# Kernel tuning notes

Hardware: AMD Instinct MI355X
Metric: run time of the kernel (lower is better)

The kernel has to match this reference:

```python
import jax, jax.numpy as jnp
import numpy as np

ITERS = 15
KERNEL = 7
PAD = 3
INIT_RATE = 0.1
SCALE_PSDF = 1000.0
EDGE_THRESH = 0.01


def _min_pool7(x):
    # torch: -maxpool2d(-x, k=7, s=1, p=3)  ==  min-pool, padding with +inf
    return jax.lax.reduce_window(
        x, jnp.inf, jax.lax.min,
        window_dimensions=(1, 1, KERNEL, KERNEL),
        window_strides=(1, 1, 1, 1),
        padding=[(0, 0), (0, 0), (PAD, PAD), (PAD, PAD)])


def _erode_weight(mask):
    # FaceWeightedFusion.obtain_face_mask_weight: 15-iter erosion, each shell
    # of pixels removed at iteration i gets weight init_rate + i*(1-init_rate)/15
    mask_erode = mask
    mask_final = jnp.zeros_like(mask)
    for i in range(ITERS):
        nxt = _min_pool7(mask_erode)
        rate = min(INIT_RATE + i * ((1.0 - INIT_RATE) / ITERS), 1.0)
        mask_final = mask_final + (mask_erode - nxt) * rate
        mask_erode = nxt
    return mask_final + mask_erode


def _bilinear_sample(img, xy):
    # img: [B,1,H,W]; xy: [B,2,N] in [-1,1] (grid_sample convention, align_corners=True)
    B, _, H, W = img.shape
    x = (xy[:, 0] + 1.0) * 0.5 * (W - 1)  # [B,N]
    y = (xy[:, 1] + 1.0) * 0.5 * (H - 1)
    x0 = jnp.floor(x); y0 = jnp.floor(y)
    wx = x - x0; wy = y - y0
    x0i = jnp.clip(x0, 0, W - 1).astype(jnp.int32)
    x1i = jnp.clip(x0 + 1, 0, W - 1).astype(jnp.int32)
    y0i = jnp.clip(y0, 0, H - 1).astype(jnp.int32)
    y1i = jnp.clip(y0 + 1, 0, H - 1).astype(jnp.int32)
    flat = img[:, 0].reshape(B, H * W)
    g = lambda yi, xi: jnp.take_along_axis(flat, yi * W + xi, axis=1)
    v = (g(y0i, x0i) * (1 - wx) * (1 - wy) + g(y0i, x1i) * wx * (1 - wy)
         + g(y1i, x0i) * (1 - wx) * wy + g(y1i, x1i) * wx * wy)
    return v[:, None, :]  # [B,1,N]


def setup_inputs() -> dict:
    key = jax.random.key(0)
    ks = jax.random.split(key, 7)
    B, H, W, N = 4, 1024, 1024, 262144
    mask = (jax.random.uniform(ks[0], (B, 1, H, W)) > 0.5).astype(jnp.float32)
    face_depth = jax.random.uniform(ks[1], (B, 1, H, W))
    face_depth_edge_mask = (jax.random.uniform(ks[2], (B, 1, H, W)) > 0.3).astype(jnp.float32)
    xy = jax.random.uniform(ks[3], (B, 2, N)) * 2.0 - 1.0
    z = jax.random.normal(ks[4], (B, 1, N)) * 0.1 + 0.5
    occ_body = jax.random.uniform(ks[5], (B, 1, N))
    occ_face = jax.random.uniform(ks[6], (B, 1, N))
    return {"mask": mask, "face_depth": face_depth,
            "face_depth_edge_mask": face_depth_edge_mask,
            "xy": xy, "z": z, "occ_body": occ_body, "occ_face": occ_face}


def reference(mask, face_depth, face_depth_edge_mask, xy, z, occ_body, occ_face):
    # obtain_face_mask_weight
    mask_erode = _erode_weight(mask)
    # calculate_fusion_weights (x_weighted=True)
    edge = _bilinear_sample(face_depth_edge_mask, xy)
    edge_b = (edge > EDGE_THRESH).astype(face_depth.dtype)
    depth_q = _bilinear_sample(face_depth, xy) * edge_b
    psdf = z - depth_q
    labels = _bilinear_sample(mask_erode, xy) * edge_b
    w = jnp.exp(-(psdf ** 2) * SCALE_PSDF) * labels
    # fusion(occ_body, occ_face)
    return w * occ_face + (1.0 - w) * occ_body
```

## Files before the change

kernel.cpp:

```cpp
#include <hip/hip_runtime.h>
#include <stdint.h>


#define HH 1024
#define WW 1024
#define HWIMG (HH * WW)
#define NPTS 262144

typedef short short2v __attribute__((ext_vector_type(2)));
typedef float f32x4 __attribute__((ext_vector_type(4)));

static __device__ __forceinline__ uint32_t umin_(uint32_t a, uint32_t b) { return a < b ? a : b; }

__global__ __launch_bounds__(256) void row_dt_kernel(const float* __restrict__ mask,
                                                     uint8_t* __restrict__ rbuf) {
    __shared__ uint64_t words[4][18];
    const int w = threadIdx.x >> 6;
    const int l = threadIdx.x & 63;
    const int row = blockIdx.x * 4 + w;
    const float* mrow = mask + (size_t)row * WW;

    if (l == 0) { words[w][0] = 0ull; words[w][17] = 0ull; }
    for (int i = 0; i < 16; ++i) {
        float m = __builtin_nontemporal_load(&mrow[i * 64 + l]);
        uint64_t bm = __ballot(m == 0.0f);
        if (l == 0) words[w][i + 1] = bm;
    }
    __syncthreads();

    uint8_t* rrow = rbuf + (size_t)row * WW;
    for (int i = 0; i < 16; ++i) {
        uint64_t W0 = words[w][i];
        uint64_t W1 = words[w][i + 1];
        uint64_t W2 = words[w][i + 2];
        uint64_t rmask = (W1 >> l) | ((W2 << 1) << (63 - l));
        uint64_t lmask = (W1 << (63 - l)) | ((W0 >> 1) >> l);
        int dr = rmask ? __builtin_ctzll(rmask) : 64;
        int dl = lmask ? __builtin_clzll(lmask) : 64;
        int d = dr < dl ? dr : dl;
        if (d > 46) d = 46;
        rrow[i * 64 + l] = (uint8_t)d;
    }
}

template<bool PACK>
__global__ __launch_bounds__(256) void col_dt_kernel(const uint8_t* __restrict__ rbuf,
                                                     const float* __restrict__ edge,
                                                     const float* __restrict__ depth,
                                                     uint8_t* __restrict__ bucket_out,
                                                     uint32_t* __restrict__ packed_out) {
    const int bx = blockIdx.x;
    const int tx = bx & 15, ty = (bx >> 4) & 15, b = bx >> 8;
    const int x0 = tx * 64, y0 = ty * 64;
    const int c = threadIdx.x & 63;
    const int t = threadIdx.x >> 6;
    const int ybase = y0 + t * 16;
    const uint8_t* img = rbuf + (size_t)b * HWIMG + x0 + c;

    uint32_t win[54];
#pragma unroll
    for (int j = 0; j < 54; ++j) {
        int r0 = ybase - 46 + 2 * j;
        int r1 = r0 + 1;
        int r0c = r0 < 0 ? 0 : (r0 > 1023 ? 1023 : r0);
        int r1c = r1 < 0 ? 0 : (r1 > 1023 ? 1023 : r1);
        uint32_t lo = img[(size_t)r0c * WW];
        uint32_t hi = img[(size_t)r1c * WW];
        if (r0 != r0c) lo = 46;
        if (r1 != r1c) hi = 46;
        win[j] = lo | (hi << 16);
    }

#pragma unroll
    for (int i = 0; i < 16; ++i) {
        const int base = i >> 1;
        const int par = i & 1;
        short2v D2 = (short2v){46, 46};
#pragma unroll
        for (int q = 0; q < 47; ++q) {
            int dy0 = 2 * q - 46 - par;
            short a0 = (short)(dy0 < 0 ? -dy0 : dy0);
            short a1 = (short)(dy0 + 1 < 0 ? -(dy0 + 1) : dy0 + 1);
            short2v A = (short2v){a0, a1};
            short2v v = __builtin_bit_cast(short2v, win[base + q]);
            short2v mx = __builtin_elementwise_max(A, v);
            D2 = __builtin_elementwise_min(D2, mx);
        }
        uint32_t D = (uint32_t)(D2.x < D2.y ? D2.x : D2.y);
        const size_t pix = (size_t)b * HWIMG + (size_t)(ybase + i) * WW + x0 + c;
        if (PACK) {
            float dv = __builtin_nontemporal_load(&depth[pix]);
            float ev = __builtin_nontemporal_load(&edge[pix]);
            uint32_t q20 = (uint32_t)fminf(rintf(dv * 1048575.0f), 1048575.0f);
            uint32_t bk = (D == 0) ? 31u : umin_(15u, (D - 1u) / 3u);
            uint32_t word = q20 | (bk << 20) | ((ev != 0.0f ? 1u : 0u) << 25);
            __builtin_nontemporal_store(word, &packed_out[pix]);
        } else {
            uint8_t o = (D == 0) ? (uint8_t)255 : (uint8_t)umin_(15u, (D - 1u) / 3u);
            bucket_out[pix] = o;
        }
    }
}

static __device__ __forceinline__ float decode_w8(uint32_t k) {
    if (k == 255u) return 0.0f;
    float v = 0.1f + (float)k * 0.06f;
    return v < 1.0f ? v : 1.0f;
}
static __device__ __forceinline__ float decode_w5(uint32_t p) {
    uint32_t k = (p >> 20) & 31u;
    if (k == 31u) return 0.0f;
    float v = 0.1f + (float)k * 0.06f;
    return v < 1.0f ? v : 1.0f;
}

__global__ __launch_bounds__(256) void sample4_kernel(
    const uint32_t* __restrict__ pimg, const float* __restrict__ xy,
    const float* __restrict__ z, const float* __restrict__ occ_body,
    const float* __restrict__ occ_face, float* __restrict__ out) {
    const int b = blockIdx.x & 3;
    const int n0 = (blockIdx.x >> 2) * 1024 + threadIdx.x * 4;
    const size_t pb = (size_t)b * NPTS;

    f32x4 xv  = __builtin_nontemporal_load((const f32x4*)&xy[pb * 2 + n0]);
    f32x4 yv  = __builtin_nontemporal_load((const f32x4*)&xy[pb * 2 + NPTS + n0]);
    f32x4 zv  = __builtin_nontemporal_load((const f32x4*)&z[pb + n0]);
    f32x4 obv = __builtin_nontemporal_load((const f32x4*)&occ_body[pb + n0]);
    f32x4 ofv = __builtin_nontemporal_load((const f32x4*)&occ_face[pb + n0]);

    const uint32_t* img = pimg + (size_t)b * HWIMG;
    f32x4 res;
    size_t idx[4][4];
    float wgt[4][4];
#pragma unroll
    for (int j = 0; j < 4; ++j) {
        float fx = ((xv[j] + 1.0f) * 0.5f) * 1023.0f;
        float fy = ((yv[j] + 1.0f) * 0.5f) * 1023.0f;
        float x0f = floorf(fx), y0f = floorf(fy);
        float wx = fx - x0f, wy = fy - y0f;
        int x0i = (int)x0f; x0i = x0i < 0 ? 0 : (x0i > 1023 ? 1023 : x0i);
        int y0i = (int)y0f; y0i = y0i < 0 ? 0 : (y0i > 1023 ? 1023 : y0i);
        int x1i = x0i + 1 > 1023 ? 1023 : x0i + 1;
        int y1i = y0i + 1 > 1023 ? 1023 : y0i + 1;
        idx[j][0] = (size_t)y0i * WW + x0i;
        idx[j][1] = (size_t)y0i * WW + x1i;
        idx[j][2] = (size_t)y1i * WW + x0i;
        idx[j][3] = (size_t)y1i * WW + x1i;
        wgt[j][0] = (1.0f - wx) * (1.0f - wy);
        wgt[j][1] = wx * (1.0f - wy);
        wgt[j][2] = (1.0f - wx) * wy;
        wgt[j][3] = wx * wy;
    }
    uint32_t pw[4][4];
#pragma unroll
    for (int j = 0; j < 4; ++j)
#pragma unroll
        for (int k = 0; k < 4; ++k) pw[j][k] = img[idx[j][k]];

#pragma unroll
    for (int j = 0; j < 4; ++j) {
        float e = (float)((pw[j][0] >> 25) & 1u) * wgt[j][0]
                + (float)((pw[j][1] >> 25) & 1u) * wgt[j][1]
                + (float)((pw[j][2] >> 25) & 1u) * wgt[j][2]
                + (float)((pw[j][3] >> 25) & 1u) * wgt[j][3];
        float w = 0.0f;
        if (e > 0.01f) {
            const float DQS = 1.0f / 1048575.0f;
            float dq = ((float)(pw[j][0] & 0xFFFFFu) * wgt[j][0]
                      + (float)(pw[j][1] & 0xFFFFFu) * wgt[j][1]
                      + (float)(pw[j][2] & 0xFFFFFu) * wgt[j][2]
                      + (float)(pw[j][3] & 0xFFFFFu) * wgt[j][3]) * DQS;
            float la = decode_w5(pw[j][0]) * wgt[j][0] + decode_w5(pw[j][1]) * wgt[j][1]
                     + decode_w5(pw[j][2]) * wgt[j][2] + decode_w5(pw[j][3]) * wgt[j][3];
            float ps = zv[j] - dq;
            w = expf(-(ps * ps) * 1000.0f) * la;
        }
        res[j] = w * ofv[j] + (1.0f - w) * obv[j];
    }
    __builtin_nontemporal_store(res, (f32x4*)&out[pb + n0]);
}

__global__ __launch_bounds__(256) void sample_fallback_kernel(
    const float* __restrict__ edge_img, const float* __restrict__ depth_img,
    const uint8_t* __restrict__ wimg,
    const float* __restrict__ xy, const float* __restrict__ z,
    const float* __restrict__ occ_body, const float* __restrict__ occ_face,
    float* __restrict__ out) {
    const int b = blockIdx.x & 3;
    const int n = (blockIdx.x >> 2) * 256 + threadIdx.x;

    float x = xy[(size_t)b * 2 * NPTS + n];
    float y = xy[(size_t)b * 2 * NPTS + NPTS + n];
    float fx = ((x + 1.0f) * 0.5f) * 1023.0f;
    float fy = ((y + 1.0f) * 0.5f) * 1023.0f;
    float x0f = floorf(fx), y0f = floorf(fy);
    float wx = fx - x0f, wy = fy - y0f;
    int x0i = (int)x0f; x0i = x0i < 0 ? 0 : (x0i > 1023 ? 1023 : x0i);
    int y0i = (int)y0f; y0i = y0i < 0 ? 0 : (y0i > 1023 ? 1023 : y0i);
    int x1i = x0i + 1 > 1023 ? 1023 : x0i + 1;
    int y1i = y0i + 1 > 1023 ? 1023 : y0i + 1;

    const size_t base = (size_t)b * HWIMG;
    const size_t i00 = base + (size_t)y0i * WW + x0i;
    const size_t i01 = base + (size_t)y0i * WW + x1i;
    const size_t i10 = base + (size_t)y1i * WW + x0i;
    const size_t i11 = base + (size_t)y1i * WW + x1i;

    const float w00 = (1.0f - wx) * (1.0f - wy);
    const float w01 = wx * (1.0f - wy);
    const float w10 = (1.0f - wx) * wy;
    const float w11 = wx * wy;

    float zv = z[(size_t)b * NPTS + n];
    float ob = occ_body[(size_t)b * NPTS + n];
    float of = occ_face[(size_t)b * NPTS + n];

    float w = 0.0f;
    float e = edge_img[i00] * w00 + edge_img[i01] * w01
            + edge_img[i10] * w10 + edge_img[i11] * w11;
    if (e > 0.01f) {
        float dq = depth_img[i00] * w00 + depth_img[i01] * w01
                 + depth_img[i10] * w10 + depth_img[i11] * w11;
        float la = decode_w8(wimg[i00]) * w00 + decode_w8(wimg[i01]) * w01
                 + decode_w8(wimg[i10]) * w10 + decode_w8(wimg[i11]) * w11;
        float ps = zv - dq;
        w = expf(-(ps * ps) * 1000.0f) * la;
    }
    out[(size_t)b * NPTS + n] = w * of + (1.0f - w) * ob;
}

extern "C" void kernel_launch(void* const* d_in, const int* in_sizes, int n_in,
                              void* d_out, int out_size, void* d_ws, size_t ws_size,
                              hipStream_t stream) {
    const float* mask      = (const float*)d_in[0];
    const float* depth     = (const float*)d_in[1];
    const float* edge      = (const float*)d_in[2];
    const float* xy        = (const float*)d_in[3];
    const float* z         = (const float*)d_in[4];
    const float* occ_body  = (const float*)d_in[5];
    const float* occ_face  = (const float*)d_in[6];
    float* out = (float*)d_out;

    uint8_t* rbuf = (uint8_t*)d_ws;
    const size_t need_packed = (size_t)4 * HWIMG + (size_t)4 * HWIMG * 4;

    row_dt_kernel<<<1024, 256, 0, stream>>>(mask, rbuf);

    if (ws_size >= need_packed) {
        uint32_t* pimg = (uint32_t*)(rbuf + (size_t)4 * HWIMG);
        col_dt_kernel<true><<<1024, 256, 0, stream>>>(rbuf, edge, depth, nullptr, pimg);
        sample4_kernel<<<1024, 256, 0, stream>>>(pimg, xy, z, occ_body, occ_face, out);
    } else {
        uint8_t* wbuf = rbuf + (size_t)4 * HWIMG;
        col_dt_kernel<false><<<1024, 256, 0, stream>>>(rbuf, edge, depth, wbuf, nullptr);
        sample_fallback_kernel<<<4096, 256, 0, stream>>>(edge, depth, wbuf,
                                                         xy, z, occ_body, occ_face, out);
    }
}
```

Measured before the change: 150.9 us.

## Fuse row and column distance transforms into one kernel using LDS tiles

```diff
diff --git a/kernel.cpp b/kernel.cpp
--- a/kernel.cpp
+++ b/kernel.cpp
@@ -6,69 +6,55 @@
 #define WW 1024
 #define HWIMG (HH * WW)
 #define NPTS 262144
+#define LSTR 156
 
 typedef short short2v __attribute__((ext_vector_type(2)));
 typedef float f32x4 __attribute__((ext_vector_type(4)));
 
 static __device__ __forceinline__ uint32_t umin_(uint32_t a, uint32_t b) { return a < b ? a : b; }
 
-__global__ __launch_bounds__(256) void row_dt_kernel(const float* __restrict__ mask,
-                                                     uint8_t* __restrict__ rbuf) {
-    __shared__ uint64_t words[4][18];
-    const int w = threadIdx.x >> 6;
-    const int l = threadIdx.x & 63;
-    const int row = blockIdx.x * 4 + w;
-    const float* mrow = mask + (size_t)row * WW;
-
-    if (l == 0) { words[w][0] = 0ull; words[w][17] = 0ull; }
-    for (int i = 0; i < 16; ++i) {
-        float m = __builtin_nontemporal_load(&mrow[i * 64 + l]);
-        uint64_t bm = __ballot(m == 0.0f);
-        if (l == 0) words[w][i + 1] = bm;
-    }
-    __syncthreads();
-
-    uint8_t* rrow = rbuf + (size_t)row * WW;
-    for (int i = 0; i < 16; ++i) {
-        uint64_t W0 = words[w][i];
-        uint64_t W1 = words[w][i + 1];
-        uint64_t W2 = words[w][i + 2];
-        uint64_t rmask = (W1 >> l) | ((W2 << 1) << (63 - l));
-        uint64_t lmask = (W1 << (63 - l)) | ((W0 >> 1) >> l);
-        int dr = rmask ? __builtin_ctzll(rmask) : 64;
-        int dl = lmask ? __builtin_clzll(lmask) : 64;
-        int d = dr < dl ? dr : dl;
-        if (d > 46) d = 46;
-        rrow[i * 64 + l] = (uint8_t)d;
-    }
-}
-
-template<bool PACK>
-__global__ __launch_bounds__(256) void col_dt_kernel(const uint8_t* __restrict__ rbuf,
-                                                     const float* __restrict__ edge,
-                                                     const float* __restrict__ depth,
-                                                     uint8_t* __restrict__ bucket_out,
-                                                     uint32_t* __restrict__ packed_out) {
+__global__ __launch_bounds__(256) void fused_dt_kernel(const float* __restrict__ mask,
+                                                       const float* __restrict__ edge,
+                                                       const float* __restrict__ depth,
+                                                       uint32_t* __restrict__ packed_out) {
+    __shared__ uint8_t lds[64 * LSTR];
     const int bx = blockIdx.x;
-    const int tx = bx & 15, ty = (bx >> 4) & 15, b = bx >> 8;
+    const int b = bx & 3;
+    const int tile = bx >> 2;
+    const int tx = tile & 15, ty = tile >> 4;
     const int x0 = tx * 64, y0 = ty * 64;
     const int c = threadIdx.x & 63;
     const int t = threadIdx.x >> 6;
+
+    const float* mimg = mask + (size_t)b * HWIMG;
+
+    for (int r = t; r < 156; r += 4) {
+        const int y = y0 - 46 + r;
+        uint32_t d = 46;
+        if (y >= 0 && y < HH) {
+            const float* mrow = mimg + (size_t)y * WW;
+            uint64_t W0 = 0, W1, W2 = 0;
+            W1 = __ballot(mrow[x0 + c] == 0.0f);
+            if (x0 > 0)        W0 = __ballot(mrow[x0 - 64 + c] == 0.0f);
+            if (x0 < WW - 64)  W2 = __ballot(mrow[x0 + 64 + c] == 0.0f);
+            uint64_t rmask = (W1 >> c) | ((W2 << 1) << (63 - c));
+            uint64_t lmask = (W1 << (63 - c)) | ((W0 >> 1) >> c);
+            int dr = rmask ? __builtin_ctzll(rmask) : 64;
+            int dl = lmask ? __builtin_clzll(lmask) : 64;
+            int dd = dr < dl ? dr : dl;
+            d = dd > 46 ? 46u : (uint32_t)dd;
+        }
+        lds[c * LSTR + r] = (uint8_t)d;
+    }
+    __syncthreads();
+
     const int ybase = y0 + t * 16;
-    const uint8_t* img = rbuf + (size_t)b * HWIMG + x0 + c;
-
+    const uint8_t* colp = lds + c * LSTR + t * 16;
     uint32_t win[54];
 #pragma unroll
     for (int j = 0; j < 54; ++j) {
-        int r0 = ybase - 46 + 2 * j;
-        int r1 = r0 + 1;
-        int r0c = r0 < 0 ? 0 : (r0 > 1023 ? 1023 : r0);
-        int r1c = r1 < 0 ? 0 : (r1 > 1023 ? 1023 : r1);
-        uint32_t lo = img[(size_t)r0c * WW];
-        uint32_t hi = img[(size_t)r1c * WW];
-        if (r0 != r0c) lo = 46;
-        if (r1 != r1c) hi = 46;
-        win[j] = lo | (hi << 16);
+        uint32_t v = *(const uint16_t*)(colp + 2 * j);
+        win[j] = (v & 0xffu) | ((v & 0xff00u) << 8);
     }
 
 #pragma unroll
@@ -88,25 +74,15 @@
         }
         uint32_t D = (uint32_t)(D2.x < D2.y ? D2.x : D2.y);
         const size_t pix = (size_t)b * HWIMG + (size_t)(ybase + i) * WW + x0 + c;
-        if (PACK) {
-            float dv = __builtin_nontemporal_load(&depth[pix]);
-            float ev = __builtin_nontemporal_load(&edge[pix]);
-            uint32_t q20 = (uint32_t)fminf(rintf(dv * 1048575.0f), 1048575.0f);
-            uint32_t bk = (D == 0) ? 31u : umin_(15u, (D - 1u) / 3u);
-            uint32_t word = q20 | (bk << 20) | ((ev != 0.0f ? 1u : 0u) << 25);
-            __builtin_nontemporal_store(word, &packed_out[pix]);
-        } else {
-            uint8_t o = (D == 0) ? (uint8_t)255 : (uint8_t)umin_(15u, (D - 1u) / 3u);
-            bucket_out[pix] = o;
-        }
-    }
-}
-
-static __device__ __forceinline__ float decode_w8(uint32_t k) {
-    if (k == 255u) return 0.0f;
-    float v = 0.1f + (float)k * 0.06f;
-    return v < 1.0f ? v : 1.0f;
-}
+        float dv = __builtin_nontemporal_load(&depth[pix]);
+        float ev = __builtin_nontemporal_load(&edge[pix]);
+        uint32_t q20 = (uint32_t)fminf(rintf(dv * 1048575.0f), 1048575.0f);
+        uint32_t bk = (D == 0) ? 31u : umin_(15u, (D - 1u) / 3u);
+        uint32_t word = q20 | (bk << 20) | ((ev != 0.0f ? 1u : 0u) << 25);
+        __builtin_nontemporal_store(word, &packed_out[pix]);
+    }
+}
+
 static __device__ __forceinline__ float decode_w5(uint32_t p) {
     uint32_t k = (p >> 20) & 31u;
     if (k == 31u) return 0.0f;
@@ -180,6 +156,87 @@
     __builtin_nontemporal_store(res, (f32x4*)&out[pb + n0]);
 }
 
+__global__ __launch_bounds__(256) void row_dt_kernel(const float* __restrict__ mask,
+                                                     uint8_t* __restrict__ rbuf) {
+    __shared__ uint64_t words[4][18];
+    const int w = threadIdx.x >> 6;
+    const int l = threadIdx.x & 63;
+    const int row = blockIdx.x * 4 + w;
+    const float* mrow = mask + (size_t)row * WW;
+
+    if (l == 0) { words[w][0] = 0ull; words[w][17] = 0ull; }
+    for (int i = 0; i < 16; ++i) {
+        float m = mrow[i * 64 + l];
+        uint64_t bm = __ballot(m == 0.0f);
+        if (l == 0) words[w][i + 1] = bm;
+    }
+    __syncthreads();
+
+    uint8_t* rrow = rbuf + (size_t)row * WW;
+    for (int i = 0; i < 16; ++i) {
+        uint64_t W0 = words[w][i];
+        uint64_t W1 = words[w][i + 1];
+        uint64_t W2 = words[w][i + 2];
+        uint64_t rmask = (W1 >> l) | ((W2 << 1) << (63 - l));
+        uint64_t lmask = (W1 << (63 - l)) | ((W0 >> 1) >> l);
+        int dr = rmask ? __builtin_ctzll(rmask) : 64;
+        int dl = lmask ? __builtin_clzll(lmask) : 64;
+        int d = dr < dl ? dr : dl;
+        if (d > 46) d = 46;
+        rrow[i * 64 + l] = (uint8_t)d;
+    }
+}
+
+__global__ __launch_bounds__(256) void col_dt_u8_kernel(const uint8_t* __restrict__ rbuf,
+                                                        uint8_t* __restrict__ bucket_out) {
+    const int bx = blockIdx.x;
+    const int tx = bx & 15, ty = (bx >> 4) & 15, b = bx >> 8;
+    const int x0 = tx * 64, y0 = ty * 64;
+    const int c = threadIdx.x & 63;
+    const int t = threadIdx.x >> 6;
+    const int ybase = y0 + t * 16;
+    const uint8_t* img = rbuf + (size_t)b * HWIMG + x0 + c;
+
+    uint32_t win[54];
+#pragma unroll
+    for (int j = 0; j < 54; ++j) {
+        int r0 = ybase - 46 + 2 * j;
+        int r1 = r0 + 1;
+        int r0c = r0 < 0 ? 0 : (r0 > 1023 ? 1023 : r0);
+        int r1c = r1 < 0 ? 0 : (r1 > 1023 ? 1023 : r1);
+        uint32_t lo = img[(size_t)r0c * WW];
+        uint32_t hi = img[(size_t)r1c * WW];
+        if (r0 != r0c) lo = 46;
+        if (r1 != r1c) hi = 46;
+        win[j] = lo | (hi << 16);
+    }
+#pragma unroll
+    for (int i = 0; i < 16; ++i) {
+        const int base = i >> 1;
+        const int par = i & 1;
+        short2v D2 = (short2v){46, 46};
+#pragma unroll
+        for (int q = 0; q < 47; ++q) {
+            int dy0 = 2 * q - 46 - par;
+            short a0 = (short)(dy0 < 0 ? -dy0 : dy0);
+            short a1 = (short)(dy0 + 1 < 0 ? -(dy0 + 1) : dy0 + 1);
+            short2v A = (short2v){a0, a1};
+            short2v v = __builtin_bit_cast(short2v, win[base + q]);
+            short2v mx = __builtin_elementwise_max(A, v);
+            D2 = __builtin_elementwise_min(D2, mx);
+        }
+        uint32_t D = (uint32_t)(D2.x < D2.y ? D2.x : D2.y);
+        uint8_t o = (D == 0) ? (uint8_t)255 : (uint8_t)umin_(15u, (D - 1u) / 3u);
+        bucket_out[(size_t)b * HWIMG + (size_t)(ybase + i) * WW + x0 + c] = o;
+    }
+}
+
+static __device__ __forceinline__ float decode_w8(uint32_t k) {
+    if (k == 255u) return 0.0f;
+    float v = 0.1f + (float)k * 0.06f;
+    return v < 1.0f ? v : 1.0f;
+}
+
 __global__ __launch_bounds__(256) void sample_fallback_kernel(
     const float* __restrict__ edge_img, const float* __restrict__ depth_img,
     const uint8_t* __restrict__ wimg,
@@ -241,18 +298,15 @@
     const float* occ_face  = (const float*)d_in[6];
     float* out = (float*)d_out;
 
-    uint8_t* rbuf = (uint8_t*)d_ws;
-    const size_t need_packed = (size_t)4 * HWIMG + (size_t)4 * HWIMG * 4;
-
-    row_dt_kernel<<<1024, 256, 0, stream>>>(mask, rbuf);
-
-    if (ws_size >= need_packed) {
-        uint32_t* pimg = (uint32_t*)(rbuf + (size_t)4 * HWIMG);
-        col_dt_kernel<true><<<1024, 256, 0, stream>>>(rbuf, edge, depth, nullptr, pimg);
+    if (ws_size >= (size_t)4 * HWIMG * 4) {
+        uint32_t* pimg = (uint32_t*)d_ws;
+        fused_dt_kernel<<<1024, 256, 0, stream>>>(mask, edge, depth, pimg);
         sample4_kernel<<<1024, 256, 0, stream>>>(pimg, xy, z, occ_body, occ_face, out);
     } else {
+        uint8_t* rbuf = (uint8_t*)d_ws;
         uint8_t* wbuf = rbuf + (size_t)4 * HWIMG;
-        col_dt_kernel<false><<<1024, 256, 0, stream>>>(rbuf, edge, depth, wbuf, nullptr);
+        row_dt_kernel<<<1024, 256, 0, stream>>>(mask, rbuf);
+        col_dt_u8_kernel<<<1024, 256, 0, stream>>>(rbuf, wbuf);
         sample_fallback_kernel<<<4096, 256, 0, stream>>>(edge, depth, wbuf,
                                                          xy, z, occ_body, occ_face, out);
     }
```

New measurement: 168.7 us. +11.8%, slower.

## Use short-radius column distance window with exact fallback; pair bilinear texel loads

Applied to the files above, without the earlier changes.

```diff
diff --git a/kernel.cpp b/kernel.cpp
--- a/kernel.cpp
+++ b/kernel.cpp
@@ -9,6 +9,7 @@
 
 typedef short short2v __attribute__((ext_vector_type(2)));
 typedef float f32x4 __attribute__((ext_vector_type(4)));
+typedef uint32_t u32x2 __attribute__((ext_vector_type(2), aligned(4)));
 
 static __device__ __forceinline__ uint32_t umin_(uint32_t a, uint32_t b) { return a < b ? a : b; }
 
@@ -22,7 +23,7 @@
 
     if (l == 0) { words[w][0] = 0ull; words[w][17] = 0ull; }
     for (int i = 0; i < 16; ++i) {
-        float m = __builtin_nontemporal_load(&mrow[i * 64 + l]);
+        float m = mrow[i * 64 + l];
         uint64_t bm = __ballot(m == 0.0f);
         if (l == 0) words[w][i + 1] = bm;
     }
@@ -55,38 +56,63 @@
     const int c = threadIdx.x & 63;
     const int t = threadIdx.x >> 6;
     const int ybase = y0 + t * 16;
-    const uint8_t* img = rbuf + (size_t)b * HWIMG + x0 + c;
-
-    uint32_t win[54];
-#pragma unroll
-    for (int j = 0; j < 54; ++j) {
-        int r0 = ybase - 46 + 2 * j;
+    const uint8_t* imgc = rbuf + (size_t)b * HWIMG + x0 + c;
+
+    uint32_t wf[12];
+#pragma unroll
+    for (int j = 0; j < 12; ++j) {
+        int r0 = ybase - 4 + 2 * j;
         int r1 = r0 + 1;
         int r0c = r0 < 0 ? 0 : (r0 > 1023 ? 1023 : r0);
         int r1c = r1 < 0 ? 0 : (r1 > 1023 ? 1023 : r1);
-        uint32_t lo = img[(size_t)r0c * WW];
-        uint32_t hi = img[(size_t)r1c * WW];
+        uint32_t lo = imgc[(size_t)r0c * WW];
+        uint32_t hi = imgc[(size_t)r1c * WW];
         if (r0 != r0c) lo = 46;
         if (r1 != r1c) hi = 46;
-        win[j] = lo | (hi << 16);
-    }
-
-#pragma unroll
-    for (int i = 0; i < 16; ++i) {
-        const int base = i >> 1;
+        wf[j] = lo | (hi << 16);
+    }
+
+    uint32_t Dv[16];
+    bool bad = false;
+#pragma unroll
+    for (int i = 0; i < 16; ++i) {
+        const int base2 = i >> 1;
         const int par = i & 1;
         short2v D2 = (short2v){46, 46};
 #pragma unroll
-        for (int q = 0; q < 47; ++q) {
-            int dy0 = 2 * q - 46 - par;
+        for (int q = 0; q < 5; ++q) {
+            int dy0 = 2 * q - 4 - par;
             short a0 = (short)(dy0 < 0 ? -dy0 : dy0);
             short a1 = (short)(dy0 + 1 < 0 ? -(dy0 + 1) : dy0 + 1);
             short2v A = (short2v){a0, a1};
-            short2v v = __builtin_bit_cast(short2v, win[base + q]);
+            short2v v = __builtin_bit_cast(short2v, wf[base2 + q]);
             short2v mx = __builtin_elementwise_max(A, v);
             D2 = __builtin_elementwise_min(D2, mx);
         }
         uint32_t D = (uint32_t)(D2.x < D2.y ? D2.x : D2.y);
+        Dv[i] = D;
+        bad |= (D >= 6);
+    }
+
+    if (__ballot(bad) != 0) {
+#pragma unroll
+        for (int i = 0; i < 16; ++i) {
+            uint32_t D = 46;
+            for (int dy = -46; dy <= 46; ++dy) {
+                int y = ybase + i + dy;
+                uint32_t r = 46;
+                if (y >= 0 && y < HH) r = imgc[(size_t)y * WW];
+                uint32_t a = (uint32_t)(dy < 0 ? -dy : dy);
+                uint32_t m = a > r ? a : r;
+                D = D < m ? D : m;
+            }
+            Dv[i] = D;
+        }
+    }
+
+#pragma unroll
+    for (int i = 0; i < 16; ++i) {
+        uint32_t D = Dv[i];
         const size_t pix = (size_t)b * HWIMG + (size_t)(ybase + i) * WW + x0 + c;
         if (PACK) {
             float dv = __builtin_nontemporal_load(&depth[pix]);
@@ -102,11 +128,6 @@
     }
 }
 
-static __device__ __forceinline__ float decode_w8(uint32_t k) {
-    if (k == 255u) return 0.0f;
-    float v = 0.1f + (float)k * 0.06f;
-    return v < 1.0f ? v : 1.0f;
-}
 static __device__ __forceinline__ float decode_w5(uint32_t p) {
     uint32_t k = (p >> 20) & 31u;
     if (k == 31u) return 0.0f;
@@ -130,7 +151,8 @@
 
     const uint32_t* img = pimg + (size_t)b * HWIMG;
     f32x4 res;
-    size_t idx[4][4];
+    const uint32_t* addr[4][2];
+    int sel[4];
     float wgt[4][4];
 #pragma unroll
     for (int j = 0; j < 4; ++j) {
@@ -140,44 +162,54 @@
         float wx = fx - x0f, wy = fy - y0f;
         int x0i = (int)x0f; x0i = x0i < 0 ? 0 : (x0i > 1023 ? 1023 : x0i);
         int y0i = (int)y0f; y0i = y0i < 0 ? 0 : (y0i > 1023 ? 1023 : y0i);
-        int x1i = x0i + 1 > 1023 ? 1023 : x0i + 1;
         int y1i = y0i + 1 > 1023 ? 1023 : y0i + 1;
-        idx[j][0] = (size_t)y0i * WW + x0i;
-        idx[j][1] = (size_t)y0i * WW + x1i;
-        idx[j][2] = (size_t)y1i * WW + x0i;
-        idx[j][3] = (size_t)y1i * WW + x1i;
+        int xl = x0i > 1022 ? 1022 : x0i;
+        sel[j] = x0i - xl;
+        addr[j][0] = img + (size_t)y0i * WW + xl;
+        addr[j][1] = img + (size_t)y1i * WW + xl;
         wgt[j][0] = (1.0f - wx) * (1.0f - wy);
         wgt[j][1] = wx * (1.0f - wy);
         wgt[j][2] = (1.0f - wx) * wy;
         wgt[j][3] = wx * wy;
     }
-    uint32_t pw[4][4];
-#pragma unroll
-    for (int j = 0; j < 4; ++j)
-#pragma unroll
-        for (int k = 0; k < 4; ++k) pw[j][k] = img[idx[j][k]];
-
+    u32x2 pr[4][2];
 #pragma unroll
     for (int j = 0; j < 4; ++j) {
-        float e = (float)((pw[j][0] >> 25) & 1u) * wgt[j][0]
-                + (float)((pw[j][1] >> 25) & 1u) * wgt[j][1]
-                + (float)((pw[j][2] >> 25) & 1u) * wgt[j][2]
-                + (float)((pw[j][3] >> 25) & 1u) * wgt[j][3];
+        pr[j][0] = *(const u32x2*)addr[j][0];
+        pr[j][1] = *(const u32x2*)addr[j][1];
+    }
+
+#pragma unroll
+    for (int j = 0; j < 4; ++j) {
+        uint32_t p00 = sel[j] ? pr[j][0].y : pr[j][0].x;
+        uint32_t p01 = pr[j][0].y;
+        uint32_t p10 = sel[j] ? pr[j][1].y : pr[j][1].x;
+        uint32_t p11 = pr[j][1].y;
+        float e = (float)((p00 >> 25) & 1u) * wgt[j][0]
+                + (float)((p01 >> 25) & 1u) * wgt[j][1]
+                + (float)((p10 >> 25) & 1u) * wgt[j][2]
+                + (float)((p11 >> 25) & 1u) * wgt[j][3];
         float w = 0.0f;
         if (e > 0.01f) {
             const float DQS = 1.0f / 1048575.0f;
-            float dq = ((float)(pw[j][0] & 0xFFFFFu) * wgt[j][0]
-                      + (float)(pw[j][1] & 0xFFFFFu) * wgt[j][1]
-                      + (float)(pw[j][2] & 0xFFFFFu) * wgt[j][2]
-                      + (float)(pw[j][3] & 0xFFFFFu) * wgt[j][3]) * DQS;
-            float la = decode_w5(pw[j][0]) * wgt[j][0] + decode_w5(pw[j][1]) * wgt[j][1]
-                     + decode_w5(pw[j][2]) * wgt[j][2] + decode_w5(pw[j][3]) * wgt[j][3];
+            float dq = ((float)(p00 & 0xFFFFFu) * wgt[j][0]
+                      + (float)(p01 & 0xFFFFFu) * wgt[j][1]
+                      + (float)(p10 & 0xFFFFFu) * wgt[j][2]
+                      + (float)(p11 & 0xFFFFFu) * wgt[j][3]) * DQS;
+            float la = decode_w5(p00) * wgt[j][0] + decode_w5(p01) * wgt[j][1]
+                     + decode_w5(p10) * wgt[j][2] + decode_w5(p11) * wgt[j][3];
             float ps = zv[j] - dq;
             w = expf(-(ps * ps) * 1000.0f) * la;
         }
         res[j] = w * ofv[j] + (1.0f - w) * obv[j];
     }
     __builtin_nontemporal_store(res, (f32x4*)&out[pb + n0]);
+}
+
+static __device__ __forceinline__ float decode_w8(uint32_t k) {
+    if (k == 255u) return 0.0f;
+    float v = 0.1f + (float)k * 0.06f;
+    return v < 1.0f ? v : 1.0f;
 }
 
 __global__ __launch_bounds__(256) void sample_fallback_kernel(
```

Result: faster. 137.4 us (-9.0%).
